# Kernel optimization log

Measured on AMD Instinct MI355X. Metric: run time of the kernel, lower is better.

The kernel has to match this reference:

```python
import jax, jax.numpy as jnp
import numpy as np

NOISE_DB = 40.0  # layer's `noise` ctor arg (SNR in dB)


def setup_inputs() -> dict:
    key = jax.random.key(0)
    k1, k2, k3 = jax.random.split(key, 3)
    B, M, L, S = 4, 256, 24, 22  # S = shots = round(M*L/(M+L-1))
    x = jax.random.normal(k1, (B, M, M, L), dtype=jnp.float32)
    # coded aperture weights, init N(0,1)/sqrt(kern*kern) as in build()
    H = jax.random.normal(k2, (1, M, M, 1, S), dtype=jnp.float32) / np.float32(M)
    # standard-normal noise sample (the layer draws this internally)
    noise_eps = jax.random.normal(k3, (B, M, M + L - 1, 1), dtype=jnp.float32)
    return {"x": x, "H": H, "noise_eps": noise_eps}


def reference(x, H, noise_eps):
    B, M, _, L = x.shape
    S = H.shape[-1]
    W = M + L - 1  # dispersed detector width
    H2 = H[0, :, :, 0, :]  # (M, M, S)

    # Aux1 = H * x : (B, M, M, L, S)
    HX = H2[None, :, :, None, :] * x[..., None]

    # Forward shear-sum: Y[b,m,n,s] = sum_i HX[b,m,n-i,i,s]
    # (equivalent to the pad + L rolls + extract-band-i + reduce_sum)
    Y = jnp.zeros((B, M, W, S), dtype=x.dtype)
    for i in range(L):  # fixed small spectral loop; indexed accumulation, no padded rolls
        Y = Y.at[:, :, i:i + M, :].add(HX[:, :, :, i, :])

    # Noise: sigma^2 = ||Y||^2 / (M * W * B * 10^(noise/10)); broadcast over shots
    sigm = jnp.sum(Y * Y) / (M * W * B * (10.0 ** (NOISE_DB / 10.0)))
    Y = Y + jnp.sqrt(sigm) * noise_eps  # noise_eps: (B, M, W, 1)

    # Reverse shift-extract: X[b,m,n,i] = sum_s H2[m,n,s] * Y[b,m,n+i,s]
    Ys = jnp.stack([Y[:, :, i:i + M, :] for i in range(L)], axis=3)  # (B,M,M,L,S)
    X = jnp.einsum('bmnls,mns->bmnl', Ys, H2)

    return X / jnp.max(X)
```

## Files before the change

kernel.cpp:

```cpp
#include <hip/hip_runtime.h>
#include <math.h>

namespace {
constexpr int Mz = 256, Lz = 24, Sz = 22, Bz = 4;
constexpr int Wz = Mz + Lz - 1;
constexpr int ST = 26;
constexpr int NBLK = Bz * Mz;
constexpr int NPASS = 7;
constexpr double SIGM_DEN = (double)Mz * (double)Wz * (double)Bz * 1e4;
}

__device__ __forceinline__ unsigned int enc_f32(float f) {
  unsigned int u = __float_as_uint(f);
  return (u & 0x80000000u) ? ~u : (u | 0x80000000u);
}
__device__ __forceinline__ float dec_f32(unsigned int e) {
  unsigned int u = (e & 0x80000000u) ? (e ^ 0x80000000u) : ~e;
  return __uint_as_float(u);
}

__device__ __forceinline__ float rot_down1(float v) {
  return __int_as_float(
      __builtin_amdgcn_update_dpp(0, __float_as_int(v), 0x130, 0xF, 0xF, true));
}

__global__ __launch_bounds__(256) void k_init(const float* __restrict__ H,
                                              float* __restrict__ hsum,
                                              double* __restrict__ sumsq,
                                              unsigned int* __restrict__ maxenc)
{
  int idx = blockIdx.x * 256 + threadIdx.x;
  if (idx == 0) { *sumsq = 0.0; *maxenc = 0u; }
  if (idx < Mz * Mz) {
    const float* __restrict__ hp = H + (size_t)idx * Sz;
    float a = 0.f;
    #pragma unroll
    for (int s = 0; s < Sz; ++s) a += hp[s];
    hsum[idx] = a;
  }
}

__global__ __launch_bounds__(256, 4) void k_fwd(const float* __restrict__ x,
                                                const float* __restrict__ H,
                                                float* __restrict__ X0,
                                                double* __restrict__ sumsq)
{
  __shared__ __align__(16) float Ys[Wz * ST];
  __shared__ double wred[4];

  const int tid = threadIdx.x;
  const int j  = tid & 63;
  const int wv = tid >> 6;
  const int b = blockIdx.x >> 8;
  const int m = blockIdx.x & 255;
  const float* __restrict__ xp = x + (size_t)(b * Mz + m) * (Mz * Lz);
  const float* __restrict__ Hp = H + (size_t)m * (Mz * Sz);

  double local = 0.0;

  for (int pp = 0; pp < 2; ++pp) {
    const int p = wv + 4 * pp;
    if (p >= NPASS) break;
    const int W0 = 41 * p;
    const int n = W0 - 23 + j;
    const bool valid = (n >= 0) && (n < Mz);

    float hr[Sz], xr[Lz];
    if (valid) {
      const float2* __restrict__ h2 = (const float2*)(Hp + n * Sz);
      #pragma unroll
      for (int k = 0; k < 11; ++k) { const float2 h = h2[k]; hr[2*k] = h.x; hr[2*k+1] = h.y; }
      const float4* __restrict__ x4 = (const float4*)(xp + n * Lz);
      #pragma unroll
      for (int k = 0; k < 6; ++k) {
        const float4 t = x4[k];
        xr[4*k] = t.x; xr[4*k+1] = t.y; xr[4*k+2] = t.z; xr[4*k+3] = t.w;
      }
    } else {
      #pragma unroll
      for (int k = 0; k < Sz; ++k) hr[k] = 0.f;
      #pragma unroll
      for (int k = 0; k < Lz; ++k) xr[k] = 0.f;
    }

    float acc[Sz];
    #pragma unroll
    for (int s = 0; s < Sz; ++s) acc[s] = 0.f;

    #pragma unroll
    for (int i = 0; i < Lz; ++i) {
      #pragma unroll
      for (int s = 0; s < Sz; ++s) acc[s] = fmaf(hr[s], xr[i], acc[s]);
      if (i < Lz - 1) {
        #pragma unroll
        for (int s = 0; s < Sz; ++s) acc[s] = rot_down1(acc[s]);
      }
    }

    const int w = W0 + j;
    if (j <= 40 && w < Wz) {
      float2* __restrict__ yrow = (float2*)&Ys[w * ST];
      #pragma unroll
      for (int k = 0; k < 11; ++k) {
        yrow[k] = make_float2(acc[2*k], acc[2*k+1]);
        local += (double)acc[2*k] * acc[2*k] + (double)acc[2*k+1] * acc[2*k+1];
      }
    }
  }

  for (int off = 32; off > 0; off >>= 1) local += __shfl_down(local, off, 64);
  const int lane = tid & 63, wid = tid >> 6;
  if (lane == 0) wred[wid] = local;
  __syncthreads();
  if (tid == 0) atomicAdd(sumsq, wred[0] + wred[1] + wred[2] + wred[3]);

  {
    const int n = tid;
    float hr[Sz];
    {
      const float2* __restrict__ h2 = (const float2*)(Hp + n * Sz);
      #pragma unroll
      for (int k = 0; k < 11; ++k) { const float2 h = h2[k]; hr[2*k] = h.x; hr[2*k+1] = h.y; }
    }
    float4* __restrict__ Xp4 =
        (float4*)(X0 + (size_t)(b * Mz + m) * (Mz * Lz) + n * Lz);
    #pragma unroll
    for (int q = 0; q < 6; ++q) {
      float o[4];
      #pragma unroll
      for (int jj = 0; jj < 4; ++jj) {
        const int l = 4 * q + jj;
        const float2* __restrict__ yr = (const float2*)&Ys[(n + l) * ST];
        float a0 = 0.f, a1 = 0.f;
        #pragma unroll
        for (int k = 0; k < 11; ++k) {
          const float2 y = yr[k];
          a0 = fmaf(y.x, hr[2*k],   a0);
          a1 = fmaf(y.y, hr[2*k+1], a1);
        }
        o[jj] = a0 + a1;
      }
      Xp4[q] = make_float4(o[0], o[1], o[2], o[3]);
    }
  }
}

__global__ __launch_bounds__(256) void k_max(const float* __restrict__ X0,
                                             const float* __restrict__ eps,
                                             const float* __restrict__ hsum,
                                             const double* __restrict__ sumsq,
                                             unsigned int* __restrict__ maxenc)
{
  const float c = sqrtf((float)(*sumsq / SIGM_DEN));
  const int n = threadIdx.x;
  const int bm = blockIdx.x;
  const int m = bm & 255;
  const float4* __restrict__ r4 = (const float4*)(X0 + (size_t)bm * (Mz * Lz) + n * Lz);
  const float* __restrict__ ep = eps + bm * Wz + n;
  const float hv = c * hsum[(m << 8) + n];

  float mx = -3.4e38f;
  #pragma unroll
  for (int q = 0; q < 6; ++q) {
    float4 t = r4[q];
    mx = fmaxf(mx, fmaf(hv, ep[4*q+0], t.x));
    mx = fmaxf(mx, fmaf(hv, ep[4*q+1], t.y));
    mx = fmaxf(mx, fmaf(hv, ep[4*q+2], t.z));
    mx = fmaxf(mx, fmaf(hv, ep[4*q+3], t.w));
  }
  for (int off = 32; off > 0; off >>= 1) mx = fmaxf(mx, __shfl_down(mx, off, 64));
  __shared__ float wredf[4];
  const int lane = n & 63, wid = n >> 6;
  if (lane == 0) wredf[wid] = mx;
  __syncthreads();
  if (n == 0) {
    float bmx = fmaxf(fmaxf(wredf[0], wredf[1]), fmaxf(wredf[2], wredf[3]));
    atomicMax(maxenc, enc_f32(bmx));
  }
}

__global__ __launch_bounds__(256) void k_final(float* __restrict__ Xio,
                                               const float* __restrict__ eps,
                                               const float* __restrict__ hsum,
                                               const double* __restrict__ sumsq,
                                               const unsigned int* __restrict__ maxenc)
{
  const float c = sqrtf((float)(*sumsq / SIGM_DEN));
  const float inv = 1.0f / dec_f32(*maxenc);
  const int n = threadIdx.x;
  const int bm = blockIdx.x;
  const int m = bm & 255;
  float4* __restrict__ r4 = (float4*)(Xio + (size_t)bm * (Mz * Lz) + n * Lz);
  const float* __restrict__ ep = eps + bm * Wz + n;
  const float hv = c * hsum[(m << 8) + n];

  #pragma unroll
  for (int q = 0; q < 6; ++q) {
    float4 t = r4[q];
    t.x = fmaf(hv, ep[4*q+0], t.x) * inv;
    t.y = fmaf(hv, ep[4*q+1], t.y) * inv;
    t.z = fmaf(hv, ep[4*q+2], t.z) * inv;
    t.w = fmaf(hv, ep[4*q+3], t.w) * inv;
    r4[q] = t;
  }
}

extern "C" void kernel_launch(void* const* d_in, const int* in_sizes, int n_in,
                              void* d_out, int out_size, void* d_ws, size_t ws_size,
                              hipStream_t stream) {
  const float* x   = (const float*)d_in[0];
  const float* H   = (const float*)d_in[1];
  const float* eps = (const float*)d_in[2];
  float* out = (float*)d_out;

  double*       sumsq  = (double*)d_ws;
  unsigned int* maxenc = (unsigned int*)((char*)d_ws + 8);
  float*        hsum   = (float*)((char*)d_ws + 16);

  k_init  <<<(Mz * Mz + 255) / 256, 256, 0, stream>>>(H, hsum, sumsq, maxenc);
  k_fwd   <<<NBLK, 256, 0, stream>>>(x, H, out, sumsq);
  k_max   <<<NBLK, 256, 0, stream>>>(out, eps, hsum, sumsq, maxenc);
  k_final <<<NBLK, 256, 0, stream>>>(out, eps, hsum, sumsq, maxenc);
}
```

Baseline: 129.4 us.

## Fold H shot-sum into forward kernel and coalesce epilogue slab accesses

```diff
diff --git a/kernel.cpp b/kernel.cpp
--- a/kernel.cpp
+++ b/kernel.cpp
@@ -24,26 +24,11 @@
       __builtin_amdgcn_update_dpp(0, __float_as_int(v), 0x130, 0xF, 0xF, true));
 }
 
-__global__ __launch_bounds__(256) void k_init(const float* __restrict__ H,
-                                              float* __restrict__ hsum,
-                                              double* __restrict__ sumsq,
-                                              unsigned int* __restrict__ maxenc)
-{
-  int idx = blockIdx.x * 256 + threadIdx.x;
-  if (idx == 0) { *sumsq = 0.0; *maxenc = 0u; }
-  if (idx < Mz * Mz) {
-    const float* __restrict__ hp = H + (size_t)idx * Sz;
-    float a = 0.f;
-    #pragma unroll
-    for (int s = 0; s < Sz; ++s) a += hp[s];
-    hsum[idx] = a;
-  }
-}
-
 __global__ __launch_bounds__(256, 4) void k_fwd(const float* __restrict__ x,
                                                 const float* __restrict__ H,
                                                 float* __restrict__ X0,
-                                                double* __restrict__ sumsq)
+                                                double* __restrict__ sumsq,
+                                                float* __restrict__ hsum)
 {
   __shared__ __align__(16) float Ys[Wz * ST];
   __shared__ double wred[4];
@@ -121,6 +106,12 @@
       const float2* __restrict__ h2 = (const float2*)(Hp + n * Sz);
       #pragma unroll
       for (int k = 0; k < 11; ++k) { const float2 h = h2[k]; hr[2*k] = h.x; hr[2*k+1] = h.y; }
+    }
+    if (b == 0) {
+      float a = 0.f;
+      #pragma unroll
+      for (int s = 0; s < Sz; ++s) a += hr[s];
+      hsum[(m << 8) + n] = a;
     }
     float4* __restrict__ Xp4 =
         (float4*)(X0 + (size_t)(b * Mz + m) * (Mz * Lz) + n * Lz);
@@ -152,28 +143,33 @@
                                              unsigned int* __restrict__ maxenc)
 {
   const float c = sqrtf((float)(*sumsq / SIGM_DEN));
-  const int n = threadIdx.x;
+  const int tid = threadIdx.x;
   const int bm = blockIdx.x;
   const int m = bm & 255;
-  const float4* __restrict__ r4 = (const float4*)(X0 + (size_t)bm * (Mz * Lz) + n * Lz);
-  const float* __restrict__ ep = eps + bm * Wz + n;
-  const float hv = c * hsum[(m << 8) + n];
+  const float4* __restrict__ slab = (const float4*)(X0 + (size_t)bm * (Mz * Lz));
+  const float* __restrict__ ep = eps + bm * Wz;
+  const float* __restrict__ hs = hsum + (m << 8);
 
   float mx = -3.4e38f;
   #pragma unroll
   for (int q = 0; q < 6; ++q) {
-    float4 t = r4[q];
-    mx = fmaxf(mx, fmaf(hv, ep[4*q+0], t.x));
-    mx = fmaxf(mx, fmaf(hv, ep[4*q+1], t.y));
-    mx = fmaxf(mx, fmaf(hv, ep[4*q+2], t.z));
-    mx = fmaxf(mx, fmaf(hv, ep[4*q+3], t.w));
+    const int idx4 = q * 256 + tid;
+    const int n = idx4 / 6;
+    const int l0 = 4 * (idx4 - 6 * n);
+    const float4 t = slab[idx4];
+    const float hv = c * hs[n];
+    const float* __restrict__ e4 = ep + n + l0;
+    mx = fmaxf(mx, fmaf(hv, e4[0], t.x));
+    mx = fmaxf(mx, fmaf(hv, e4[1], t.y));
+    mx = fmaxf(mx, fmaf(hv, e4[2], t.z));
+    mx = fmaxf(mx, fmaf(hv, e4[3], t.w));
   }
   for (int off = 32; off > 0; off >>= 1) mx = fmaxf(mx, __shfl_down(mx, off, 64));
   __shared__ float wredf[4];
-  const int lane = n & 63, wid = n >> 6;
+  const int lane = tid & 63, wid = tid >> 6;
   if (lane == 0) wredf[wid] = mx;
   __syncthreads();
-  if (n == 0) {
+  if (tid == 0) {
     float bmx = fmaxf(fmaxf(wredf[0], wredf[1]), fmaxf(wredf[2], wredf[3]));
     atomicMax(maxenc, enc_f32(bmx));
   }
@@ -187,21 +183,26 @@
 {
   const float c = sqrtf((float)(*sumsq / SIGM_DEN));
   const float inv = 1.0f / dec_f32(*maxenc);
-  const int n = threadIdx.x;
+  const int tid = threadIdx.x;
   const int bm = blockIdx.x;
   const int m = bm & 255;
-  float4* __restrict__ r4 = (float4*)(Xio + (size_t)bm * (Mz * Lz) + n * Lz);
-  const float* __restrict__ ep = eps + bm * Wz + n;
-  const float hv = c * hsum[(m << 8) + n];
+  float4* __restrict__ slab = (float4*)(Xio + (size_t)bm * (Mz * Lz));
+  const float* __restrict__ ep = eps + bm * Wz;
+  const float* __restrict__ hs = hsum + (m << 8);
 
   #pragma unroll
   for (int q = 0; q < 6; ++q) {
-    float4 t = r4[q];
-    t.x = fmaf(hv, ep[4*q+0], t.x) * inv;
-    t.y = fmaf(hv, ep[4*q+1], t.y) * inv;
-    t.z = fmaf(hv, ep[4*q+2], t.z) * inv;
-    t.w = fmaf(hv, ep[4*q+3], t.w) * inv;
-    r4[q] = t;
+    const int idx4 = q * 256 + tid;
+    const int n = idx4 / 6;
+    const int l0 = 4 * (idx4 - 6 * n);
+    float4 t = slab[idx4];
+    const float hv = c * hs[n];
+    const float* __restrict__ e4 = ep + n + l0;
+    t.x = fmaf(hv, e4[0], t.x) * inv;
+    t.y = fmaf(hv, e4[1], t.y) * inv;
+    t.z = fmaf(hv, e4[2], t.z) * inv;
+    t.w = fmaf(hv, e4[3], t.w) * inv;
+    slab[idx4] = t;
   }
 }
 
@@ -217,8 +218,8 @@
   unsigned int* maxenc = (unsigned int*)((char*)d_ws + 8);
   float*        hsum   = (float*)((char*)d_ws + 16);
 
-  k_init  <<<(Mz * Mz + 255) / 256, 256, 0, stream>>>(H, hsum, sumsq, maxenc);
-  k_fwd   <<<NBLK, 256, 0, stream>>>(x, H, out, sumsq);
+  hipMemsetAsync(d_ws, 0, 16, stream);
+  k_fwd   <<<NBLK, 256, 0, stream>>>(x, H, out, sumsq, hsum);
   k_max   <<<NBLK, 256, 0, stream>>>(out, eps, hsum, sumsq, maxenc);
   k_final <<<NBLK, 256, 0, stream>>>(out, eps, hsum, sumsq, maxenc);
 }
```

New measurement: 124.3 us. -3.9%, faster.
